# Performance work log

Measured on AMD Instinct MI355X. Metric: run time of the kernel, lower is better.

Reference implementation:

```python
import jax, jax.numpy as jnp
import numpy as np

B, T, OUT, IN, H = 128, 512, 256, 1024, 1024  # batch, seq_len, output_size, hidden_size(lstm in), input_size(lstm hidden)


def lstm_layer(x_seq, Wih, Whh, bih, bhh):
    """Single LSTM layer, PyTorch gate order (i, f, g, o).
    x_seq: [B, T, In] -> h_seq: [B, T, H]"""
    # input contribution is independent of the recurrence: compute once
    gx = jnp.einsum('bti,gi->btg', x_seq, Wih) + bih  # [B, T, 4H]
    gx = jnp.swapaxes(gx, 0, 1)  # [T, B, 4H] for scan over time
    Hh = Whh.shape[1]

    def step(carry, gxt):
        h, c = carry
        gates = gxt + h @ Whh.T + bhh  # [B, 4H]
        i, f, g, o = jnp.split(gates, 4, axis=-1)
        i = jax.nn.sigmoid(i)
        f = jax.nn.sigmoid(f)
        g = jnp.tanh(g)
        o = jax.nn.sigmoid(o)
        c = f * c + i * g
        h = o * jnp.tanh(c)
        return (h, c), h

    h0 = jnp.zeros((x_seq.shape[0], Hh), dtype=x_seq.dtype)
    c0 = jnp.zeros_like(h0)
    _, hs = jax.lax.scan(step, (h0, c0), gx)
    return jnp.swapaxes(hs, 0, 1)  # [B, T, H]


def setup_inputs() -> dict:
    key = jax.random.key(0)
    ks = jax.random.split(key, 12)
    s_fc = 1.0 / np.sqrt(OUT)
    s_l = 1.0 / np.sqrt(H)
    inp = {
        'x': jax.random.normal(ks[0], (B, OUT), dtype=jnp.float32),
        'fc_w': jax.random.uniform(ks[1], (IN, OUT), jnp.float32, -s_fc, s_fc),
        'fc_b': jax.random.uniform(ks[2], (IN,), jnp.float32, -s_fc, s_fc),
        'Wih0': jax.random.uniform(ks[3], (4 * H, IN), jnp.float32, -s_l, s_l),
        'Whh0': jax.random.uniform(ks[4], (4 * H, H), jnp.float32, -s_l, s_l),
        'bih0': jax.random.uniform(ks[5], (4 * H,), jnp.float32, -s_l, s_l),
        'bhh0': jax.random.uniform(ks[6], (4 * H,), jnp.float32, -s_l, s_l),
        'Wih1': jax.random.uniform(ks[7], (4 * H, H), jnp.float32, -s_l, s_l),
        'Whh1': jax.random.uniform(ks[8], (4 * H, H), jnp.float32, -s_l, s_l),
        'bih1': jax.random.uniform(ks[9], (4 * H,), jnp.float32, -s_l, s_l),
        'bhh1': jax.random.uniform(ks[10], (4 * H,), jnp.float32, -s_l, s_l),
    }
    return inp


def reference(x, fc_w, fc_b, Wih0, Whh0, bih0, bhh0, Wih1, Whh1, bih1, bhh1):
    # fc + (eval-mode) dropout, then broadcast the constant input across time
    z = x @ fc_w.T + fc_b  # [B, IN]
    z_seq = jnp.broadcast_to(z[:, None, :], (z.shape[0], T, z.shape[1]))  # [B, T, IN]
    h1 = lstm_layer(z_seq, Wih0, Whh0, bih0, bhh0)  # [B, T, H]
    # inter-layer dropout is identity in eval mode
    h2 = lstm_layer(h1, Wih1, Whh1, bih1, bhh1)  # [B, T, H]
    return h2
```

## Files before the change

kernel.cpp:

```cpp
#include <hip/hip_runtime.h>

typedef __attribute__((ext_vector_type(8))) short bf16x8;
typedef __attribute__((ext_vector_type(4))) float f32x4;
typedef unsigned short u16;
typedef unsigned long long u64;

#define T_SEQ 512
#define NBLK  192
#define FPAD  16

__device__ __forceinline__ u16 f2bf(float f) {
  unsigned int u = __float_as_uint(f);
  u += 0x7fffu + ((u >> 16) & 1u);
  return (u16)(u >> 16);
}
__device__ __forceinline__ float sigm_(float x) { return 1.f / (1.f + __expf(-x)); }
__device__ __forceinline__ float tanh_(float x) { return 1.f - 2.f / (__expf(2.f * x) + 1.f); }

template <typename T>
__device__ __forceinline__ void st_agent(T* p, T v) {
  __hip_atomic_store(p, v, __ATOMIC_RELAXED, __HIP_MEMORY_SCOPE_AGENT);
}
template <typename T>
__device__ __forceinline__ T ld_agent(const T* p) {
  return __hip_atomic_load(p, __ATOMIC_RELAXED, __HIP_MEMORY_SCOPE_AGENT);
}
__device__ __forceinline__ u64 pack2f(float a, float b) {
  return (u64)__float_as_uint(a) | ((u64)__float_as_uint(b) << 32);
}
__device__ __forceinline__ u64 pack4bf(f32x4 v) {
  return (u64)f2bf(v[0]) | ((u64)f2bf(v[1]) << 16) |
         ((u64)f2bf(v[2]) << 32) | ((u64)f2bf(v[3]) << 48);
}

__global__ void fc_kernel(const float* __restrict__ x, const float* __restrict__ w,
                          const float* __restrict__ bias, float* __restrict__ z) {
  int idx = blockIdx.x * 256 + threadIdx.x;
  int b = idx >> 10, i = idx & 1023;
  const float* xr = x + b * 256;
  const float* wr = w + i * 256;
  float acc = bias[i];
  #pragma unroll 4
  for (int o = 0; o < 256; ++o) acc += xr[o] * wr[o];
  z[idx] = acc;
}

__global__ void gx0_kernel(const float* __restrict__ z, const float* __restrict__ Wih0,
                           const float* __restrict__ bih, const float* __restrict__ bhh,
                           float* __restrict__ gx0) {
  int idx = blockIdx.x * 256 + threadIdx.x;
  int b = idx >> 12, j = idx & 4095;
  const float* zr = z + b * 1024;
  const float* wr = Wih0 + (size_t)j * 1024;
  float acc = bih[j] + bhh[j];
  #pragma unroll 4
  for (int k = 0; k < 1024; ++k) acc += zr[k] * wr[k];
  gx0[idx] = acc;
}

__global__ __launch_bounds__(512, 2)
void lstm_persist(const float* __restrict__ Whh0, const float* __restrict__ Wih1,
                  const float* __restrict__ Whh1, const float* __restrict__ gx0,
                  const float* __restrict__ bih1, const float* __restrict__ bhh1,
                  u16* __restrict__ h0ring, u16* __restrict__ h1ring,
                  float* __restrict__ pabuf, float* __restrict__ out,
                  int* __restrict__ flags, int* __restrict__ epoch) {
  __shared__ __align__(16) u16 wlds[4][2048][8];
  __shared__ __align__(16) float red[4][64][16];
  __shared__ __align__(16) float stage[128][16];

  const int bid = blockIdx.x;
  const int role = bid >> 6;
  const int cslice = bid & 63;
  const int cb = cslice * 16;
  const int tid = threadIdx.x;
  const int w = tid >> 6;
  const int lane = tid & 63;
  const int l15 = lane & 15;
  const int q = lane >> 4;
  const int Mg = w & 3;
  const int kh = w >> 2;

  {
    const float* Wsrc = (role == 0) ? Whh0 : (role == 1) ? Wih1 : Whh1;
    const int r = tid >> 3;
    const int g = r >> 4, n = r & 15;
    const int k0 = (tid & 7) * 128;
    const float* src = Wsrc + (((size_t)(g * 1024 + cb + n)) << 10) + k0;
    for (int k = 0; k < 128; k += 4) {
      float4 v = *(const float4*)(src + k);
      ushort4 o;
      o.x = f2bf(v.x); o.y = f2bf(v.y); o.z = f2bf(v.z); o.w = f2bf(v.w);
      const int kk = k0 + k;
      *(ushort4*)&wlds[g][((kk >> 3) << 4) + n][kk & 7] = o;
    }
  }

  float c_st[2][4];
  #pragma unroll
  for (int mt = 0; mt < 2; ++mt)
    #pragma unroll
    for (int r = 0; r < 4; ++r) c_st[mt][r] = 0.f;

  float gx[2][4][4];
  float b1[4];
  if (role == 0 && w < 4) {
    #pragma unroll
    for (int mt = 0; mt < 2; ++mt)
      #pragma unroll
      for (int g = 0; g < 4; ++g)
        #pragma unroll
        for (int r = 0; r < 4; ++r)
          gx[mt][g][r] = gx0[(size_t)(w * 32 + mt * 16 + q * 4 + r) * 4096 + g * 1024 + cb + l15];
  }
  if (role == 2 && w < 4) {
    #pragma unroll
    for (int g = 0; g < 4; ++g)
      b1[g] = bih1[g * 1024 + cb + l15] + bhh1[g * 1024 + cb + l15];
  }
  __syncthreads();

  const size_t HSLOT = (size_t)128 * 1024;

  for (int p = 0; p < T_SEQ + 2; ++p) {
    const int t = p - role;
    if (t >= 0 && t < T_SEQ) {
      const u16* A;
      if (role == 1)      A = h0ring + (size_t)(t & 1) * HSLOT;
      else if (role == 0) A = h0ring + (size_t)((t + 1) & 1) * HSLOT;
      else                A = h1ring + (size_t)((t + 1) & 1) * HSLOT;

      const int kbase = kh * 512;
      const u16* Ap = A + (((size_t)(Mg * 32 + l15)) << 10) + kbase + q * 8;
      const int cellbase = ((kbase >> 3) + q) * 16 + l15;

      f32x4 acc0[4] = {{0.f,0.f,0.f,0.f},{0.f,0.f,0.f,0.f},{0.f,0.f,0.f,0.f},{0.f,0.f,0.f,0.f}};
      f32x4 acc1[4] = {{0.f,0.f,0.f,0.f},{0.f,0.f,0.f,0.f},{0.f,0.f,0.f,0.f},{0.f,0.f,0.f,0.f}};

      #pragma unroll
      for (int kk = 0; kk < 16; ++kk) {
        bf16x8 a0 = *(const bf16x8*)(Ap + kk * 32);
        bf16x8 a1 = *(const bf16x8*)(Ap + (16 << 10) + kk * 32);
        #pragma unroll
        for (int g = 0; g < 4; ++g) {
          bf16x8 b = *(const bf16x8*)&wlds[g][cellbase + kk * 64][0];
          acc0[g] = __builtin_amdgcn_mfma_f32_16x16x32_bf16(a0, b, acc0[g], 0, 0, 0);
          acc1[g] = __builtin_amdgcn_mfma_f32_16x16x32_bf16(a1, b, acc1[g], 0, 0, 0);
        }
      }

      u64 pa64[16];
      const float* pr = pabuf + (size_t)(t & 1) * 524288 + (size_t)(cslice * 4 + w) * 2048;
      if (role == 2 && w < 4) {
        #pragma unroll
        for (int j = 0; j < 8; ++j) {
          pa64[j * 2]     = ld_agent((const u64*)pr + j * 128 + lane * 2);
          pa64[j * 2 + 1] = ld_agent((const u64*)pr + j * 128 + lane * 2 + 1);
        }
      }

      if (w >= 4) {
        #pragma unroll
        for (int g = 0; g < 4; ++g) *(f32x4*)&red[w - 4][lane][g * 4] = acc0[g];
      }
      __syncthreads();
      if (w < 4) {
        #pragma unroll
        for (int g = 0; g < 4; ++g) acc0[g] += *(const f32x4*)&red[w][lane][g * 4];
      }
      __syncthreads();
      if (w >= 4) {
        #pragma unroll
        for (int g = 0; g < 4; ++g) *(f32x4*)&red[w - 4][lane][g * 4] = acc1[g];
      }
      __syncthreads();
      if (w < 4) {
        #pragma unroll
        for (int g = 0; g < 4; ++g) acc1[g] += *(const f32x4*)&red[w][lane][g * 4];

        if (role == 1) {
          float* pw = pabuf + (size_t)(t & 1) * 524288 + (size_t)(cslice * 4 + w) * 2048;
          #pragma unroll
          for (int g = 0; g < 4; ++g) {
            st_agent((u64*)pw + g * 128 + lane * 2,           pack2f(acc0[g][0], acc0[g][1]));
            st_agent((u64*)pw + g * 128 + lane * 2 + 1,       pack2f(acc0[g][2], acc0[g][3]));
            st_agent((u64*)pw + (4 + g) * 128 + lane * 2,     pack2f(acc1[g][0], acc1[g][1]));
            st_agent((u64*)pw + (4 + g) * 128 + lane * 2 + 1, pack2f(acc1[g][2], acc1[g][3]));
          }
        } else {
          #pragma unroll
          for (int mt = 0; mt < 2; ++mt) {
            #pragma unroll
            for (int r = 0; r < 4; ++r) {
              float xi, xf, xg, xo;
              f32x4* a = mt ? acc1 : acc0;
              if (role == 0) {
                xi = a[0][r] + gx[mt][0][r];
                xf = a[1][r] + gx[mt][1][r];
                xg = a[2][r] + gx[mt][2][r];
                xo = a[3][r] + gx[mt][3][r];
              } else {
                const int h2 = r >> 1, lo = r & 1;
                auto up = [&](int j) {
                  u64 v = pa64[j * 2 + h2];
                  return __uint_as_float(lo ? (unsigned)(v >> 32) : (unsigned)v);
                };
                xi = a[0][r] + up(mt * 4 + 0) + b1[0];
                xf = a[1][r] + up(mt * 4 + 1) + b1[1];
                xg = a[2][r] + up(mt * 4 + 2) + b1[2];
                xo = a[3][r] + up(mt * 4 + 3) + b1[3];
              }
              float i_ = sigm_(xi), f_ = sigm_(xf), g_ = tanh_(xg), o_ = sigm_(xo);
              float cn = f_ * c_st[mt][r] + i_ * g_;
              c_st[mt][r] = cn;
              float h = o_ * tanh_(cn);
              stage[w * 32 + mt * 16 + q * 4 + r][l15] = h;
            }
          }
        }
      }

      if (role != 1) {
        __syncthreads();
        const int row = tid >> 2, qt = tid & 3;
        f32x4 v = *(const f32x4*)&stage[row][qt * 4];
        u64 pk = pack4bf(v);
        if (role == 0) {
          st_agent((u64*)(h0ring + (size_t)(t & 1) * HSLOT + ((size_t)row << 10) + cb) + qt, pk);
        } else {
          st_agent((u64*)(h1ring + (size_t)(t & 1) * HSLOT + ((size_t)row << 10) + cb) + qt, pk);
          *(f32x4*)(out + (size_t)row * ((size_t)T_SEQ * 1024) + (size_t)t * 1024 + cb + qt * 4) = v;
        }
      }
    }

    __syncthreads();
    const int need = p + 1;
    if (tid == 0) st_agent(flags + bid * FPAD, need);
    if (bid == 0 && w == 0) {
      bool ok;
      do {
        int f0 = ld_agent(flags + lane * FPAD);
        int f1 = ld_agent(flags + (64 + lane) * FPAD);
        int f2 = ld_agent(flags + (128 + lane) * FPAD);
        ok = __all(min(f0, min(f1, f2)) >= need);
        if (!ok) __builtin_amdgcn_s_sleep(1);
      } while (!ok);
      st_agent(epoch + lane * FPAD, need);
      st_agent(epoch + (64 + lane) * FPAD, need);
      st_agent(epoch + (128 + lane) * FPAD, need);
    }
    if (tid == 0) {
      while (ld_agent(epoch + bid * FPAD) < need) __builtin_amdgcn_s_sleep(1);
      __builtin_amdgcn_fence(__ATOMIC_ACQUIRE, "agent");
    }
    __syncthreads();
  }
}

extern "C" void kernel_launch(void* const* d_in, const int* in_sizes, int n_in,
                              void* d_out, int out_size, void* d_ws, size_t ws_size,
                              hipStream_t stream) {
  (void)in_sizes; (void)n_in; (void)out_size; (void)ws_size;
  const float* x    = (const float*)d_in[0];
  const float* fc_w = (const float*)d_in[1];
  const float* fc_b = (const float*)d_in[2];
  const float* Wih0 = (const float*)d_in[3];
  const float* Whh0 = (const float*)d_in[4];
  const float* bih0 = (const float*)d_in[5];
  const float* bhh0 = (const float*)d_in[6];
  const float* Wih1 = (const float*)d_in[7];
  const float* Whh1 = (const float*)d_in[8];
  const float* bih1 = (const float*)d_in[9];
  const float* bhh1 = (const float*)d_in[10];
  float* out = (float*)d_out;

  char* ws = (char*)d_ws;
  size_t off = 0;
  auto alloc = [&](size_t bytes) -> void* {
    void* p = ws + off;
    off += (bytes + 255) & ~(size_t)255;
    return p;
  };
  float* z      = (float*)alloc((size_t)128 * 1024 * 4);
  float* gx0    = (float*)alloc((size_t)128 * 4096 * 4);
  u16*   h0ring = (u16*)alloc((size_t)2 * 128 * 1024 * 2);
  u16*   h1ring = (u16*)alloc((size_t)2 * 128 * 1024 * 2);
  float* pabuf  = (float*)alloc((size_t)2 * 524288 * 4);
  int*   flags  = (int*)alloc(NBLK * FPAD * 4);
  int*   epoch  = (int*)alloc(NBLK * FPAD * 4);

  hipMemsetAsync(h0ring, 0, (size_t)2 * 128 * 1024 * 2, stream);
  hipMemsetAsync(h1ring, 0, (size_t)2 * 128 * 1024 * 2, stream);
  hipMemsetAsync(flags, 0, NBLK * FPAD * 4, stream);
  hipMemsetAsync(epoch, 0, NBLK * FPAD * 4, stream);

  fc_kernel<<<512, 256, 0, stream>>>(x, fc_w, fc_b, z);
  gx0_kernel<<<2048, 256, 0, stream>>>(z, Wih0, bih0, bhh0, gx0);

  lstm_persist<<<NBLK, 512, 0, stream>>>(Whh0, Wih1, Whh1, gx0, bih1, bhh1,
                                         h0ring, h1ring, pabuf, out, flags, epoch);
}
```

Baseline: 7.539 ms.

## Replace global barrier with per-slot dataflow flags and 4-deep ring buffers

Drops the centralized grid-wide barrier, where block 0 gathered every flag and broadcast an epoch. Each role now waits only on the producer flags it actually depends on, using 4-slot rings for h0, h1 and the partial-activation buffer so the three roles can run several steps apart. This removes the barrier's serialization and lets layer-0, the input projection and layer-1 pipeline loosely. It also pads the LDS reduction and staging arrays to cut bank conflicts. The cost is more intricate flag logic, with a risk of ordering or deadlock bugs.

```diff
diff --git a/kernel.cpp b/kernel.cpp
--- a/kernel.cpp
+++ b/kernel.cpp
@@ -8,6 +8,7 @@
 #define T_SEQ 512
 #define NBLK  192
 #define FPAD  16
+#define RSLOT 4
 
 __device__ __forceinline__ u16 f2bf(float f) {
   unsigned int u = __float_as_uint(f);
@@ -64,10 +65,11 @@
                   const float* __restrict__ bih1, const float* __restrict__ bhh1,
                   u16* __restrict__ h0ring, u16* __restrict__ h1ring,
                   float* __restrict__ pabuf, float* __restrict__ out,
-                  int* __restrict__ flags, int* __restrict__ epoch) {
+                  int* __restrict__ h0flag, int* __restrict__ paflag,
+                  int* __restrict__ h1flag) {
   __shared__ __align__(16) u16 wlds[4][2048][8];
-  __shared__ __align__(16) float red[4][64][16];
-  __shared__ __align__(16) float stage[128][16];
+  __shared__ __align__(16) float red[4][64][20];
+  __shared__ __align__(16) float stage[128][20];
 
   const int bid = blockIdx.x;
   const int role = bid >> 6;
@@ -122,139 +124,153 @@
 
   const size_t HSLOT = (size_t)128 * 1024;
 
-  for (int p = 0; p < T_SEQ + 2; ++p) {
-    const int t = p - role;
-    if (t >= 0 && t < T_SEQ) {
-      const u16* A;
-      if (role == 1)      A = h0ring + (size_t)(t & 1) * HSLOT;
-      else if (role == 0) A = h0ring + (size_t)((t + 1) & 1) * HSLOT;
-      else                A = h1ring + (size_t)((t + 1) & 1) * HSLOT;
-
-      const int kbase = kh * 512;
-      const u16* Ap = A + (((size_t)(Mg * 32 + l15)) << 10) + kbase + q * 8;
-      const int cellbase = ((kbase >> 3) + q) * 16 + l15;
-
-      f32x4 acc0[4] = {{0.f,0.f,0.f,0.f},{0.f,0.f,0.f,0.f},{0.f,0.f,0.f,0.f},{0.f,0.f,0.f,0.f}};
-      f32x4 acc1[4] = {{0.f,0.f,0.f,0.f},{0.f,0.f,0.f,0.f},{0.f,0.f,0.f,0.f},{0.f,0.f,0.f,0.f}};
-
-      #pragma unroll
-      for (int kk = 0; kk < 16; ++kk) {
-        bf16x8 a0 = *(const bf16x8*)(Ap + kk * 32);
-        bf16x8 a1 = *(const bf16x8*)(Ap + (16 << 10) + kk * 32);
+  for (int t = 0; t < T_SEQ; ++t) {
+    const int sA = (t + 3) & 3;
+    const int sW = t & 3;
+
+    if (w == 0) {
+      bool ok;
+      if (role == 0) {
+        do {
+          int fa = ld_agent(h0flag + (sA * 64 + lane) * FPAD);
+          int fb = ld_agent(paflag + (sW * 64 + lane) * FPAD);
+          ok = __all(fa >= t && fb >= t - 3);
+          if (!ok) __builtin_amdgcn_s_sleep(1);
+        } while (!ok);
+      } else if (role == 1) {
+        do {
+          int fa = ld_agent(h0flag + (sW * 64 + lane) * FPAD);
+          int fb = (lane == 0) ? ld_agent(h1flag + (sW * 64 + cslice) * FPAD)
+                               : 0x7fffffff;
+          ok = __all(fa >= t + 1 && fb >= t - 3);
+          if (!ok) __builtin_amdgcn_s_sleep(1);
+        } while (!ok);
+      } else {
+        do {
+          int fa = ld_agent(h1flag + (sA * 64 + lane) * FPAD);
+          int fb = (lane == 0) ? ld_agent(paflag + (sW * 64 + cslice) * FPAD)
+                               : 0x7fffffff;
+          ok = __all(fa >= t && fb >= t + 1);
+          if (!ok) __builtin_amdgcn_s_sleep(1);
+        } while (!ok);
+      }
+      __builtin_amdgcn_fence(__ATOMIC_ACQUIRE, "agent");
+    }
+    __syncthreads();
+
+    const u16* A = (role == 0) ? h0ring + (size_t)sA * HSLOT
+                 : (role == 1) ? h0ring + (size_t)sW * HSLOT
+                               : h1ring + (size_t)sA * HSLOT;
+
+    const int kbase = kh * 512;
+    const u16* Ap = A + (((size_t)(Mg * 32 + l15)) << 10) + kbase + q * 8;
+    const int cellbase = ((kbase >> 3) + q) * 16 + l15;
+
+    f32x4 acc0[4] = {{0.f,0.f,0.f,0.f},{0.f,0.f,0.f,0.f},{0.f,0.f,0.f,0.f},{0.f,0.f,0.f,0.f}};
+    f32x4 acc1[4] = {{0.f,0.f,0.f,0.f},{0.f,0.f,0.f,0.f},{0.f,0.f,0.f,0.f},{0.f,0.f,0.f,0.f}};
+
+    #pragma unroll
+    for (int kk = 0; kk < 16; ++kk) {
+      bf16x8 a0 = *(const bf16x8*)(Ap + kk * 32);
+      bf16x8 a1 = *(const bf16x8*)(Ap + (16 << 10) + kk * 32);
+      #pragma unroll
+      for (int g = 0; g < 4; ++g) {
+        bf16x8 b = *(const bf16x8*)&wlds[g][cellbase + kk * 64][0];
+        acc0[g] = __builtin_amdgcn_mfma_f32_16x16x32_bf16(a0, b, acc0[g], 0, 0, 0);
+        acc1[g] = __builtin_amdgcn_mfma_f32_16x16x32_bf16(a1, b, acc1[g], 0, 0, 0);
+      }
+    }
+
+    u64 pa64[16];
+    const float* pr = pabuf + (size_t)sW * 524288 + (size_t)(cslice * 4 + w) * 2048;
+    if (role == 2 && w < 4) {
+      #pragma unroll
+      for (int j = 0; j < 8; ++j) {
+        pa64[j * 2]     = ld_agent((const u64*)pr + j * 128 + lane * 2);
+        pa64[j * 2 + 1] = ld_agent((const u64*)pr + j * 128 + lane * 2 + 1);
+      }
+    }
+
+    if (w >= 4) {
+      #pragma unroll
+      for (int g = 0; g < 4; ++g) *(f32x4*)&red[w - 4][lane][g * 4] = acc0[g];
+    }
+    __syncthreads();
+    if (w < 4) {
+      #pragma unroll
+      for (int g = 0; g < 4; ++g) acc0[g] += *(const f32x4*)&red[w][lane][g * 4];
+    }
+    __syncthreads();
+    if (w >= 4) {
+      #pragma unroll
+      for (int g = 0; g < 4; ++g) *(f32x4*)&red[w - 4][lane][g * 4] = acc1[g];
+    }
+    __syncthreads();
+    if (w < 4) {
+      #pragma unroll
+      for (int g = 0; g < 4; ++g) acc1[g] += *(const f32x4*)&red[w][lane][g * 4];
+
+      if (role == 1) {
+        float* pw = pabuf + (size_t)sW * 524288 + (size_t)(cslice * 4 + w) * 2048;
         #pragma unroll
         for (int g = 0; g < 4; ++g) {
-          bf16x8 b = *(const bf16x8*)&wlds[g][cellbase + kk * 64][0];
-          acc0[g] = __builtin_amdgcn_mfma_f32_16x16x32_bf16(a0, b, acc0[g], 0, 0, 0);
-          acc1[g] = __builtin_amdgcn_mfma_f32_16x16x32_bf16(a1, b, acc1[g], 0, 0, 0);
+          st_agent((u64*)pw + g * 128 + lane * 2,           pack2f(acc0[g][0], acc0[g][1]));
+          st_agent((u64*)pw + g * 128 + lane * 2 + 1,       pack2f(acc0[g][2], acc0[g][3]));
+          st_agent((u64*)pw + (4 + g) * 128 + lane * 2,     pack2f(acc1[g][0], acc1[g][1]));
+          st_agent((u64*)pw + (4 + g) * 128 + lane * 2 + 1, pack2f(acc1[g][2], acc1[g][3]));
         }
-      }
-
-      u64 pa64[16];
-      const float* pr = pabuf + (size_t)(t & 1) * 524288 + (size_t)(cslice * 4 + w) * 2048;
-      if (role == 2 && w < 4) {
+      } else {
         #pragma unroll
-        for (int j = 0; j < 8; ++j) {
-          pa64[j * 2]     = ld_agent((const u64*)pr + j * 128 + lane * 2);
-          pa64[j * 2 + 1] = ld_agent((const u64*)pr + j * 128 + lane * 2 + 1);
-        }
-      }
-
-      if (w >= 4) {
-        #pragma unroll
-        for (int g = 0; g < 4; ++g) *(f32x4*)&red[w - 4][lane][g * 4] = acc0[g];
-      }
-      __syncthreads();
-      if (w < 4) {
-        #pragma unroll
-        for (int g = 0; g < 4; ++g) acc0[g] += *(const f32x4*)&red[w][lane][g * 4];
-      }
-      __syncthreads();
-      if (w >= 4) {
-        #pragma unroll
-        for (int g = 0; g < 4; ++g) *(f32x4*)&red[w - 4][lane][g * 4] = acc1[g];
-      }
-      __syncthreads();
-      if (w < 4) {
-        #pragma unroll
-        for (int g = 0; g < 4; ++g) acc1[g] += *(const f32x4*)&red[w][lane][g * 4];
-
-        if (role == 1) {
-          float* pw = pabuf + (size_t)(t & 1) * 524288 + (size_t)(cslice * 4 + w) * 2048;
+        for (int mt = 0; mt < 2; ++mt) {
           #pragma unroll
-          for (int g = 0; g < 4; ++g) {
-            st_agent((u64*)pw + g * 128 + lane * 2,           pack2f(acc0[g][0], acc0[g][1]));
-            st_agent((u64*)pw + g * 128 + lane * 2 + 1,       pack2f(acc0[g][2], acc0[g][3]));
-            st_agent((u64*)pw + (4 + g) * 128 + lane * 2,     pack2f(acc1[g][0], acc1[g][1]));
-            st_agent((u64*)pw + (4 + g) * 128 + lane * 2 + 1, pack2f(acc1[g][2], acc1[g][3]));
-          }
-        } else {
-          #pragma unroll
-          for (int mt = 0; mt < 2; ++mt) {
-            #pragma unroll
-            for (int r = 0; r < 4; ++r) {
-              float xi, xf, xg, xo;
-              f32x4* a = mt ? acc1 : acc0;
-              if (role == 0) {
-                xi = a[0][r] + gx[mt][0][r];
-                xf = a[1][r] + gx[mt][1][r];
-                xg = a[2][r] + gx[mt][2][r];
-                xo = a[3][r] + gx[mt][3][r];
-              } else {
-                const int h2 = r >> 1, lo = r & 1;
-                auto up = [&](int j) {
-                  u64 v = pa64[j * 2 + h2];
-                  return __uint_as_float(lo ? (unsigned)(v >> 32) : (unsigned)v);
-                };
-                xi = a[0][r] + up(mt * 4 + 0) + b1[0];
-                xf = a[1][r] + up(mt * 4 + 1) + b1[1];
-                xg = a[2][r] + up(mt * 4 + 2) + b1[2];
-                xo = a[3][r] + up(mt * 4 + 3) + b1[3];
-              }
-              float i_ = sigm_(xi), f_ = sigm_(xf), g_ = tanh_(xg), o_ = sigm_(xo);
-              float cn = f_ * c_st[mt][r] + i_ * g_;
-              c_st[mt][r] = cn;
-              float h = o_ * tanh_(cn);
-              stage[w * 32 + mt * 16 + q * 4 + r][l15] = h;
+          for (int r = 0; r < 4; ++r) {
+            float xi, xf, xg, xo;
+            f32x4* a = mt ? acc1 : acc0;
+            if (role == 0) {
+              xi = a[0][r] + gx[mt][0][r];
+              xf = a[1][r] + gx[mt][1][r];
+              xg = a[2][r] + gx[mt][2][r];
+              xo = a[3][r] + gx[mt][3][r];
+            } else {
+              const int h2 = r >> 1, lo = r & 1;
+              auto up = [&](int j) {
+                u64 v = pa64[j * 2 + h2];
+                return __uint_as_float(lo ? (unsigned)(v >> 32) : (unsigned)v);
+              };
+              xi = a[0][r] + up(mt * 4 + 0) + b1[0];
+              xf = a[1][r] + up(mt * 4 + 1) + b1[1];
+              xg = a[2][r] + up(mt * 4 + 2) + b1[2];
+              xo = a[3][r] + up(mt * 4 + 3) + b1[3];
             }
+            float i_ = sigm_(xi), f_ = sigm_(xf), g_ = tanh_(xg), o_ = sigm_(xo);
+            float cn = f_ * c_st[mt][r] + i_ * g_;
+            c_st[mt][r] = cn;
+            float h = o_ * tanh_(cn);
+            stage[w * 32 + mt * 16 + q * 4 + r][l15] = h;
           }
         }
       }
-
-      if (role != 1) {
-        __syncthreads();
-        const int row = tid >> 2, qt = tid & 3;
-        f32x4 v = *(const f32x4*)&stage[row][qt * 4];
-        u64 pk = pack4bf(v);
-        if (role == 0) {
-          st_agent((u64*)(h0ring + (size_t)(t & 1) * HSLOT + ((size_t)row << 10) + cb) + qt, pk);
-        } else {
-          st_agent((u64*)(h1ring + (size_t)(t & 1) * HSLOT + ((size_t)row << 10) + cb) + qt, pk);
-          *(f32x4*)(out + (size_t)row * ((size_t)T_SEQ * 1024) + (size_t)t * 1024 + cb + qt * 4) = v;
-        }
-      }
-    }
-
-    __syncthreads();
-    const int need = p + 1;
-    if (tid == 0) st_agent(flags + bid * FPAD, need);
-    if (bid == 0 && w == 0) {
-      bool ok;
-      do {
-        int f0 = ld_agent(flags + lane * FPAD);
-        int f1 = ld_agent(flags + (64 + lane) * FPAD);
-        int f2 = ld_agent(flags + (128 + lane) * FPAD);
-        ok = __all(min(f0, min(f1, f2)) >= need);
-        if (!ok) __builtin_amdgcn_s_sleep(1);
-      } while (!ok);
-      st_agent(epoch + lane * FPAD, need);
-      st_agent(epoch + (64 + lane) * FPAD, need);
-      st_agent(epoch + (128 + lane) * FPAD, need);
-    }
+    }
+
+    if (role != 1) {
+      __syncthreads();
+      const int row = tid >> 2, qt = tid & 3;
+      f32x4 v = *(const f32x4*)&stage[row][qt * 4];
+      u64 pk = pack4bf(v);
+      if (role == 0) {
+        st_agent((u64*)(h0ring + (size_t)sW * HSLOT + ((size_t)row << 10) + cb) + qt, pk);
+      } else {
+        st_agent((u64*)(h1ring + (size_t)sW * HSLOT + ((size_t)row << 10) + cb) + qt, pk);
+        *(f32x4*)(out + (size_t)row * ((size_t)T_SEQ * 1024) + (size_t)t * 1024 + cb + qt * 4) = v;
+      }
+    }
+
+    __syncthreads();
     if (tid == 0) {
-      while (ld_agent(epoch + bid * FPAD) < need) __builtin_amdgcn_s_sleep(1);
-      __builtin_amdgcn_fence(__ATOMIC_ACQUIRE, "agent");
-    }
-    __syncthreads();
+      if (role == 0)      st_agent(h0flag + (sW * 64 + cslice) * FPAD, t + 1);
+      else if (role == 1) st_agent(paflag + (sW * 64 + cslice) * FPAD, t + 1);
+      else                st_agent(h1flag + (sW * 64 + cslice) * FPAD, t + 1);
+    }
   }
 }
 
@@ -284,20 +300,23 @@
   };
   float* z      = (float*)alloc((size_t)128 * 1024 * 4);
   float* gx0    = (float*)alloc((size_t)128 * 4096 * 4);
-  u16*   h0ring = (u16*)alloc((size_t)2 * 128 * 1024 * 2);
-  u16*   h1ring = (u16*)alloc((size_t)2 * 128 * 1024 * 2);
-  float* pabuf  = (float*)alloc((size_t)2 * 524288 * 4);
-  int*   flags  = (int*)alloc(NBLK * FPAD * 4);
-  int*   epoch  = (int*)alloc(NBLK * FPAD * 4);
-
-  hipMemsetAsync(h0ring, 0, (size_t)2 * 128 * 1024 * 2, stream);
-  hipMemsetAsync(h1ring, 0, (size_t)2 * 128 * 1024 * 2, stream);
-  hipMemsetAsync(flags, 0, NBLK * FPAD * 4, stream);
-  hipMemsetAsync(epoch, 0, NBLK * FPAD * 4, stream);
+  u16*   h0ring = (u16*)alloc((size_t)RSLOT * 128 * 1024 * 2);
+  u16*   h1ring = (u16*)alloc((size_t)RSLOT * 128 * 1024 * 2);
+  float* pabuf  = (float*)alloc((size_t)RSLOT * 524288 * 4);
+  int*   h0flag = (int*)alloc((size_t)RSLOT * 64 * FPAD * 4);
+  int*   paflag = (int*)alloc((size_t)RSLOT * 64 * FPAD * 4);
+  int*   h1flag = (int*)alloc((size_t)RSLOT * 64 * FPAD * 4);
+
+  hipMemsetAsync(h0ring, 0, (size_t)RSLOT * 128 * 1024 * 2, stream);
+  hipMemsetAsync(h1ring, 0, (size_t)RSLOT * 128 * 1024 * 2, stream);
+  hipMemsetAsync(h0flag, 0, (size_t)RSLOT * 64 * FPAD * 4, stream);
+  hipMemsetAsync(paflag, 0, (size_t)RSLOT * 64 * FPAD * 4, stream);
+  hipMemsetAsync(h1flag, 0, (size_t)RSLOT * 64 * FPAD * 4, stream);
 
   fc_kernel<<<512, 256, 0, stream>>>(x, fc_w, fc_b, z);
   gx0_kernel<<<2048, 256, 0, stream>>>(z, Wih0, bih0, bhh0, gx0);
 
   lstm_persist<<<NBLK, 512, 0, stream>>>(Whh0, Wih1, Whh1, gx0, bih1, bhh1,
-                                         h0ring, h1ring, pabuf, out, flags, epoch);
-}
+                                         h0ring, h1ring, pabuf, out,
+                                         h0flag, paflag, h1flag);
+}
```

Measured after the change: 6.998 ms. 1.08x faster.
